# Kernel tuning notes

Measured on AMD Instinct MI355X. Metric: run time of the kernel, lower is better.

Reference implementation:

```python
import jax, jax.numpy as jnp
import numpy as np

B, S, H = 64, 512, 768      # batch, subtokens, BERT hidden
N, E = 128, 1024            # word-nodes per graph, directed edges per graph
GH, FH, L = 128, 256, 2     # gnn_hidden, fc_hidden, num_labels


def setup_inputs() -> dict:
    key = jax.random.key(0)
    ks = jax.random.split(key, 14)
    p = lambda k, shp: 0.02 * jax.random.normal(k, shp, jnp.float32)
    return {
        "last_hidden": jax.random.normal(ks[0], (B, S, H), jnp.float32),
        "submap": jax.random.randint(ks[1], (B, S), 0, N, dtype=jnp.int32),
        "edge_index": jax.random.randint(ks[2], (B, 2, E), 0, N, dtype=jnp.int32),
        "num_nodes": N,
        "wr": p(ks[3], (H,)), "br": jnp.zeros((), jnp.float32),
        "W1": p(ks[4], (H, GH)), "b1": jnp.zeros((GH,), jnp.float32),
        "W2": p(ks[5], (GH, GH)), "b2": jnp.zeros((GH,), jnp.float32),
        "Wf1": p(ks[6], (H + GH, FH)), "bf1": jnp.zeros((FH,), jnp.float32),
        "Wf2": p(ks[7], (FH, L)), "bf2": jnp.zeros((L,), jnp.float32),
    }


def reference(last_hidden, submap, edge_index, num_nodes,
              wr, br, W1, b1, W2, b2, Wf1, bf1, Wf2, bf2):
    Bn, Sn, Hn = last_hidden.shape
    Nn = num_nodes
    BN = Bn * Nn

    # --- per-token rationale gating ---
    gate = jax.nn.sigmoid(jnp.einsum("bsh,h->bs", last_hidden, wr) + br)  # [B,S]
    gated = last_hidden * gate[..., None]                                  # [B,S,H]

    # --- subtoken -> word-node mean pooling (batched segment mean) ---
    offs = (jnp.arange(Bn, dtype=submap.dtype) * Nn)[:, None]
    seg = (submap + offs).reshape(-1)                     # [B*S] global node ids
    flat = gated.reshape(Bn * Sn, Hn)
    sums = jax.ops.segment_sum(flat, seg, num_segments=BN)
    cnts = jax.ops.segment_sum(jnp.ones((Bn * Sn,), flat.dtype), seg, num_segments=BN)
    node_feats = sums / jnp.maximum(cnts, 1.0)[:, None]   # zeros where no subtoken maps

    # --- batched GCN message passing (self-loops + PyG gcn_norm) ---
    eoffs = (jnp.arange(Bn, dtype=edge_index.dtype) * Nn)[:, None]
    src = (edge_index[:, 0, :] + eoffs).reshape(-1)       # [B*E]
    dst = (edge_index[:, 1, :] + eoffs).reshape(-1)
    self_idx = jnp.arange(BN, dtype=src.dtype)
    src_all = jnp.concatenate([src, self_idx])
    dst_all = jnp.concatenate([dst, self_idx])
    deg = jax.ops.segment_sum(jnp.ones_like(src_all, jnp.float32), dst_all, num_segments=BN)
    dinv = jax.lax.rsqrt(deg)                             # deg >= 1 due to self-loops
    norm = dinv[src_all] * dinv[dst_all]                  # [B*E + B*N]

    def gcn_layer(x, W, b):
        h = x @ W                                         # transform first (PyG GCNConv)
        msg = h[src_all] * norm[:, None]
        out = jax.ops.segment_sum(msg, dst_all, num_segments=BN) + b
        return jax.nn.relu(out)                           # relu applied in forward()

    x = gcn_layer(node_feats, W1, b1)
    x = gcn_layer(x, W2, b2)

    # --- graph mean pool, concat with CLS, classifier head (dropout = eval identity) ---
    pooled = x.reshape(Bn, Nn, -1).mean(axis=1)           # [B,GH]
    cls_emb = last_hidden[:, 0, :]                        # [B,H]
    h = jax.nn.relu(jnp.concatenate([cls_emb, pooled], axis=1) @ Wf1 + bf1)
    return h @ Wf2 + bf2                                  # [B,num_labels]
```

## Files before the change

kernel.cpp:

```cpp
#include <hip/hip_runtime.h>
#include <math.h>

#define Bz 64
#define Sz 512
#define Hz 768
#define Nz 128
#define Ez 1024
#define GHz 128
#define FHz 256
#define Lz 2
#define BNz (Bz * Nz)

typedef short bf16x8 __attribute__((ext_vector_type(8)));
typedef float f32x4  __attribute__((ext_vector_type(4)));
typedef unsigned short ushort;

__device__ inline ushort f2b(float f) {
    union { float f; unsigned u; } v; v.f = f;
    return (ushort)((v.u + 0x7FFFu + ((v.u >> 16) & 1u)) >> 16);
}

__global__ __launch_bounds__(256) void k_stage(
        const float* __restrict__ lh, const int* __restrict__ submap,
        const float* __restrict__ wr, const float* __restrict__ br,
        const float* __restrict__ W1, const float* __restrict__ W2,
        const int* __restrict__ ei, const float* __restrict__ Wf1,
        ushort* __restrict__ nfb, ushort* __restrict__ W1T, ushort* __restrict__ W2T,
        int* __restrict__ rowptrG, int* __restrict__ srcsG,
        float* __restrict__ wnG, float* __restrict__ dinvG,
        float* __restrict__ redA_G) {
    int blk = blockIdx.x, t = threadIdx.x;
    __shared__ __align__(16) char arena[17408];

    if (blk < 64) {
        int b = blk;
        float* clsL = (float*)arena;
        float* pA   = (float*)(arena + 3072);
        clsL[t]       = lh[(size_t)b * Sz * Hz + t];
        clsL[t + 256] = lh[(size_t)b * Sz * Hz + t + 256];
        clsL[t + 512] = lh[(size_t)b * Sz * Hz + t + 512];
        __syncthreads();
        int f2 = t & 127, kc = t >> 7;
        const float* Wp = Wf1 + (size_t)(kc * 384) * FHz + f2 * 2;
        const float* ip = clsL + kc * 384;
        float ax = 0.f, ay = 0.f;
        #pragma unroll 8
        for (int k = 0; k < 384; ++k) {
            float iv = ip[k];
            float2 wv = *(const float2*)&Wp[(size_t)k * FHz];
            ax += iv * wv.x; ay += iv * wv.y;
        }
        pA[kc * 256 + f2 * 2]     = ax;
        pA[kc * 256 + f2 * 2 + 1] = ay;
        __syncthreads();
        if (t < 128) {
            float2 o;
            o.x = pA[2 * t]     + pA[256 + 2 * t];
            o.y = pA[2 * t + 1] + pA[256 + 2 * t + 1];
            *(float2*)&redA_G[b * 256 + 2 * t] = o;
        }
        return;
    }
    if (blk < 78) {
        ushort* sT = (ushort*)arena;
        bool isW2 = (blk >= 76);
        int T = isW2 ? (blk - 76) : (blk - 64);
        int k0 = T * 64;
        const float* Wsrc = isW2 ? W2 : W1;
        #pragma unroll
        for (int j = 0; j < 32; ++j) {
            int idx = j * 256 + t;
            int k = idx >> 7, n = idx & 127;
            sT[k * 136 + n] = f2b(Wsrc[(size_t)(k0 + k) * 128 + n]);
        }
        __syncthreads();
        if (isW2) {
            #pragma unroll
            for (int j = 0; j < 32; ++j) {
                int idx = j * 256 + t;
                int n = idx >> 6, k = idx & 63;
                W2T[n * GHz + k0 + k] = sT[k * 136 + n];
            }
        } else {
            #pragma unroll
            for (int j = 0; j < 32; ++j) {
                int idx = j * 256 + t;
                int n = idx >> 6, k = idx & 63;
                W1T[n * Hz + k0 + k] = sT[k * 136 + n];
            }
        }
        return;
    }
    if (blk < 142) {
        int b = blk - 78;
        int*   srcl2 = (int*)arena;
        int*   dstl2 = (int*)(arena + 4096);
        int*   hist  = (int*)(arena + 8192);
        int*   off   = (int*)(arena + 8704);
        int*   rp    = (int*)(arena + 9216);
        float* di    = (float*)(arena + 9732);
        if (t < Nz) { hist[t] = 0; off[t] = 0; }
        __syncthreads();
        #pragma unroll
        for (int j = 0; j < 4; ++j) {
            int e = t + 256 * j;
            int s = ei[b * 2 * Ez + e], d = ei[b * 2 * Ez + Ez + e];
            srcl2[e] = s; dstl2[e] = d;
            atomicAdd(&hist[d], 1);
        }
        __syncthreads();
        if (t < Nz) {
            di[t] = rsqrtf((float)hist[t] + 1.0f);
            dinvG[b * Nz + t] = di[t];
        }
        __syncthreads();
        if (t < 64) {
            int s0 = hist[2 * t], s1 = hist[2 * t + 1];
            int tot = s0 + s1, run = tot;
            #pragma unroll
            for (int o = 1; o < 64; o <<= 1) {
                int v = __shfl_up(run, o);
                if (t >= o) run += v;
            }
            int excl = run - tot;
            rp[2 * t] = excl; rp[2 * t + 1] = excl + s0;
            if (t == 63) rp[Nz] = run;
        }
        __syncthreads();
        #pragma unroll
        for (int j = 0; j < 4; ++j) {
            int e = t + 256 * j;
            int s = srcl2[e], d = dstl2[e];
            int pos = rp[d] + atomicAdd(&off[d], 1);
            srcsG[b * Ez + pos] = s;
            wnG[b * Ez + pos] = di[s] * di[d];
        }
        if (t < Nz) rowptrG[b * (Nz + 1) + t] = rp[t];
        if (t == 0) rowptrG[b * (Nz + 1) + Nz] = rp[Nz];
        return;
    }

    int g = blk - 142;
    int b = g >> 7, n = g & 127;
    int lane = t & 63, wid = t >> 6;
    float* partial = (float*)arena;
    int*   list    = (int*)(arena + 9216);
    int*   lcnt    = (int*)(arena + 11264);
    if (t == 0) *lcnt = 0;
    __syncthreads();
    #pragma unroll
    for (int j = 0; j < 2; ++j) {
        int s = t + 256 * j;
        if (submap[b * Sz + s] == n) { int p = atomicAdd(lcnt, 1); list[p] = s; }
    }
    __syncthreads();
    int cnt = *lcnt;
    float brv = br[0];
    const float* wp = wr + lane * 12;
    float4 w0 = *(const float4*)&wp[0];
    float4 w1 = *(const float4*)&wp[4];
    float4 w2 = *(const float4*)&wp[8];
    float4 a0 = {0,0,0,0}, a1 = {0,0,0,0}, a2 = {0,0,0,0};
    for (int i = wid; i < cnt; i += 4) {
        const float* x = lh + (size_t)(b * Sz + list[i]) * Hz + lane * 12;
        float4 v0 = *(const float4*)&x[0];
        float4 v1 = *(const float4*)&x[4];
        float4 v2 = *(const float4*)&x[8];
        float p = v0.x*w0.x + v0.y*w0.y + v0.z*w0.z + v0.w*w0.w
                + v1.x*w1.x + v1.y*w1.y + v1.z*w1.z + v1.w*w1.w
                + v2.x*w2.x + v2.y*w2.y + v2.z*w2.z + v2.w*w2.w;
        #pragma unroll
        for (int o = 32; o > 0; o >>= 1) p += __shfl_down(p, o);
        float z = __shfl(p, 0) + brv;
        float g2 = 1.0f / (1.0f + __expf(-z));
        a0.x += g2*v0.x; a0.y += g2*v0.y; a0.z += g2*v0.z; a0.w += g2*v0.w;
        a1.x += g2*v1.x; a1.y += g2*v1.y; a1.z += g2*v1.z; a1.w += g2*v1.w;
        a2.x += g2*v2.x; a2.y += g2*v2.y; a2.z += g2*v2.z; a2.w += g2*v2.w;
    }
    if (wid > 0) {
        float* pp = partial + (wid - 1) * Hz + lane * 12;
        *(float4*)&pp[0] = a0; *(float4*)&pp[4] = a1; *(float4*)&pp[8] = a2;
    }
    __syncthreads();
    if (wid == 0) {
        float invc = 1.0f / fmaxf((float)cnt, 1.0f);
        #pragma unroll
        for (int m = 0; m < 3; ++m) {
            const float* pp = partial + m * Hz + lane * 12;
            float4 p0 = *(const float4*)&pp[0];
            float4 p1 = *(const float4*)&pp[4];
            float4 p2 = *(const float4*)&pp[8];
            a0.x += p0.x; a0.y += p0.y; a0.z += p0.z; a0.w += p0.w;
            a1.x += p1.x; a1.y += p1.y; a1.z += p1.z; a1.w += p1.w;
            a2.x += p2.x; a2.y += p2.y; a2.z += p2.z; a2.w += p2.w;
        }
        float o[12];
        o[0]=a0.x*invc; o[1]=a0.y*invc; o[2]=a0.z*invc;  o[3]=a0.w*invc;
        o[4]=a1.x*invc; o[5]=a1.y*invc; o[6]=a1.z*invc;  o[7]=a1.w*invc;
        o[8]=a2.x*invc; o[9]=a2.y*invc; o[10]=a2.z*invc; o[11]=a2.w*invc;
        unsigned* ob = (unsigned*)(nfb + (size_t)(b * Nz + n) * Hz + lane * 12);
        #pragma unroll
        for (int j = 0; j < 6; ++j)
            ob[j] = (unsigned)f2b(o[2*j]) | ((unsigned)f2b(o[2*j+1]) << 16);
    }
}

#define GSP 72
#define O_BS    18432
#define O_HL    36864
#define O_XB    102400
#define O_RP    137216
#define O_SRC   137744
#define O_WN    141840
#define O_DIL   145936
#define O_POOL  146448
#define O_HVEC  146960
__global__ __launch_bounds__(1024) void k_gnn_fused(
        const ushort* __restrict__ nfb, const ushort* __restrict__ W1T,
        const ushort* __restrict__ W2T,
        const int* __restrict__ rowptrG, const int* __restrict__ srcsG,
        const float* __restrict__ wnG, const float* __restrict__ dinvG,
        const float* __restrict__ b1, const float* __restrict__ b2,
        const float* __restrict__ redA_G,
        const float* __restrict__ Wf1, const float* __restrict__ bf1,
        const float* __restrict__ Wf2, const float* __restrict__ bf2,
        float* __restrict__ outG) {
    __shared__ __align__(16) char Lar[147984];
    ushort* As   = (ushort*)(Lar);
    ushort* Bs   = (ushort*)(Lar + O_BS);
    ushort* W2s  = (ushort*)(Lar);
    float*  hLf  = (float*)(Lar + O_HL);
    ushort* xb   = (ushort*)(Lar + O_XB);
    float*  wsum = (float*)(Lar + O_XB);
    float*  redB = (float*)(Lar + O_XB + 8192);
    int*    rp   = (int*)(Lar + O_RP);
    int*    srcl = (int*)(Lar + O_SRC);
    float*  wnl  = (float*)(Lar + O_WN);
    float*  dil  = (float*)(Lar + O_DIL);
    float*  pooledL = (float*)(Lar + O_POOL);
    float*  hvecL   = (float*)(Lar + O_HVEC);
    const float2* hL2 = (const float2*)hLf;

    int b = blockIdx.x;
    int t = threadIdx.x;
    int w = t >> 6, lane = t & 63;
    int q = lane >> 4, l16 = lane & 15;
    int wm = w >> 2, wn2 = w & 3;
    int kq = q * 8;
    int ar = t >> 3, as_ = t & 7;

    const ushort* Ab = nfb + (size_t)b * Nz * Hz;
    uint4 aA, bA, aB, bB;
    aA = *(const uint4*)&Ab[(size_t)ar * Hz + 0  + as_ * 8];
    bA = *(const uint4*)&W1T[(size_t)ar * Hz + 0  + as_ * 8];
    aB = *(const uint4*)&Ab[(size_t)ar * Hz + 64 + as_ * 8];
    bB = *(const uint4*)&W1T[(size_t)ar * Hz + 64 + as_ * 8];
    __builtin_amdgcn_sched_barrier(0);

    if (t < Nz + 1) rp[t] = rowptrG[b * (Nz + 1) + t];
    if (t < Nz) dil[t] = dinvG[b * Nz + t];
    srcl[t] = srcsG[b * Ez + t];
    wnl[t]  = wnG[b * Ez + t];

    f32x4 acc00 = {0,0,0,0}, acc01 = {0,0,0,0}, acc10 = {0,0,0,0}, acc11 = {0,0,0,0};
    auto mfma_tile = [&]() {
        #pragma unroll
        for (int ks = 0; ks < 64; ks += 32) {
            bf16x8 af0 = *(const bf16x8*)&As[(wm * 32 +      l16) * GSP + ks + kq];
            bf16x8 af1 = *(const bf16x8*)&As[(wm * 32 + 16 + l16) * GSP + ks + kq];
            bf16x8 bv0 = *(const bf16x8*)&Bs[(wn2 * 32 +      l16) * GSP + ks + kq];
            bf16x8 bv1 = *(const bf16x8*)&Bs[(wn2 * 32 + 16 + l16) * GSP + ks + kq];
            acc00 = __builtin_amdgcn_mfma_f32_16x16x32_bf16(af0, bv0, acc00, 0, 0, 0);
            acc01 = __builtin_amdgcn_mfma_f32_16x16x32_bf16(af0, bv1, acc01, 0, 0, 0);
            acc10 = __builtin_amdgcn_mfma_f32_16x16x32_bf16(af1, bv0, acc10, 0, 0, 0);
            acc11 = __builtin_amdgcn_mfma_f32_16x16x32_bf16(af1, bv1, acc11, 0, 0, 0);
        }
    };

    for (int k0 = 0; k0 < Hz; k0 += 128) {
        __syncthreads();
        *(uint4*)&As[ar * GSP + as_ * 8] = aA;
        *(uint4*)&Bs[ar * GSP + as_ * 8] = bA;
        if (k0 + 128 < Hz) {
            aA = *(const uint4*)&Ab[(size_t)ar * Hz + k0 + 128 + as_ * 8];
            bA = *(const uint4*)&W1T[(size_t)ar * Hz + k0 + 128 + as_ * 8];
        }
        __builtin_amdgcn_sched_barrier(0);
        __syncthreads();
        mfma_tile();
        __syncthreads();
        *(uint4*)&As[ar * GSP + as_ * 8] = aB;
        *(uint4*)&Bs[ar * GSP + as_ * 8] = bB;
        if (k0 + 192 < Hz) {
            aB = *(const uint4*)&Ab[(size_t)ar * Hz + k0 + 192 + as_ * 8];
            bB = *(const uint4*)&W1T[(size_t)ar * Hz + k0 + 192 + as_ * 8];
        }
        __builtin_amdgcn_sched_barrier(0);
        __syncthreads();
        mfma_tile();
    }
    {
        int c0 = wn2 * 32 + l16, c1 = c0 + 16;
        #pragma unroll
        for (int r = 0; r < 4; ++r) {
            int r0 = (wm * 32 + q * 4 + r) * 128, r1 = r0 + 16 * 128;
            hLf[r0 + (c0 & 63) * 2 + (c0 >> 6)] = acc00[r];
            hLf[r0 + (c1 & 63) * 2 + (c1 >> 6)] = acc01[r];
            hLf[r1 + (c0 & 63) * 2 + (c0 >> 6)] = acc10[r];
            hLf[r1 + (c1 & 63) * 2 + (c1 >> 6)] = acc11[r];
        }
    }
    __syncthreads();

    int n0 = t >> 4, sg = t & 15;
    uint4 w2r0 = *(const uint4*)&W2T[n0 * GHz + sg * 8];
    uint4 w2r1 = *(const uint4*)&W2T[(n0 + 64) * GHz + sg * 8];
    __builtin_amdgcn_sched_barrier(0);

    float bx0 = b1[lane], bx1 = b1[lane + 64];
    for (int d = w; d < Nz; d += 16) {
        float dd = dil[d];
        float2 hv = hL2[d * 64 + lane];
        float a0 = hv.x * dd * dd, a1 = hv.y * dd * dd;
        float c0 = 0.f, c1 = 0.f;
        int i = rp[d], pe = rp[d + 1];
        for (; i + 4 <= pe; i += 4) {
            int s0_ = srcl[i], s1_ = srcl[i+1], s2_ = srcl[i+2], s3_ = srcl[i+3];
            float m0 = wnl[i], m1 = wnl[i+1], m2 = wnl[i+2], m3 = wnl[i+3];
            float2 h0 = hL2[s0_ * 64 + lane], h1 = hL2[s1_ * 64 + lane];
            float2 h2 = hL2[s2_ * 64 + lane], h3 = hL2[s3_ * 64 + lane];
            a0 += h0.x*m0; a1 += h0.y*m0; c0 += h1.x*m1; c1 += h1.y*m1;
            a0 += h2.x*m2; a1 += h2.y*m2; c0 += h3.x*m3; c1 += h3.y*m3;
        }
        for (; i < pe; ++i) {
            int s_ = srcl[i]; float nm = wnl[i];
            float2 h = hL2[s_ * 64 + lane];
            a0 += h.x * nm; a1 += h.y * nm;
        }
        a0 += c0; a1 += c1;
        xb[d * 136 + lane]      = f2b(fmaxf(a0 + bx0, 0.0f));
        xb[d * 136 + lane + 64] = f2b(fmaxf(a1 + bx1, 0.0f));
    }
    __syncthreads();

    *(uint4*)((char*)W2s + n0 * 272 + sg * 16)        = w2r0;
    *(uint4*)((char*)W2s + (n0 + 64) * 272 + sg * 16) = w2r1;
    __syncthreads();

    acc00 = (f32x4){0,0,0,0}; acc01 = (f32x4){0,0,0,0};
    acc10 = (f32x4){0,0,0,0}; acc11 = (f32x4){0,0,0,0};
    #pragma unroll
    for (int ks = 0; ks < GHz; ks += 32) {
        bf16x8 af0 = *(const bf16x8*)&xb[(wm * 32 +      l16) * 136 + ks + kq];
        bf16x8 af1 = *(const bf16x8*)&xb[(wm * 32 + 16 + l16) * 136 + ks + kq];
        bf16x8 bv0 = *(const bf16x8*)&W2s[(wn2 * 32 +      l16) * 136 + ks + kq];
        bf16x8 bv1 = *(const bf16x8*)&W2s[(wn2 * 32 + 16 + l16) * 136 + ks + kq];
        acc00 = __builtin_amdgcn_mfma_f32_16x16x32_bf16(af0, bv0, acc00, 0, 0, 0);
        acc01 = __builtin_amdgcn_mfma_f32_16x16x32_bf16(af0, bv1, acc01, 0, 0, 0);
        acc10 = __builtin_amdgcn_mfma_f32_16x16x32_bf16(af1, bv0, acc10, 0, 0, 0);
        acc11 = __builtin_amdgcn_mfma_f32_16x16x32_bf16(af1, bv1, acc11, 0, 0, 0);
    }
    __syncthreads();
    {
        int c0 = wn2 * 32 + l16, c1 = c0 + 16;
        #pragma unroll
        for (int r = 0; r < 4; ++r) {
            int r0 = (wm * 32 + q * 4 + r) * 128, r1 = r0 + 16 * 128;
            hLf[r0 + (c0 & 63) * 2 + (c0 >> 6)] = acc00[r];
            hLf[r0 + (c1 & 63) * 2 + (c1 >> 6)] = acc01[r];
            hLf[r1 + (c0 & 63) * 2 + (c0 >> 6)] = acc10[r];
            hLf[r1 + (c1 & 63) * 2 + (c1 >> 6)] = acc11[r];
        }
    }
    __syncthreads();

    float by0 = b2[lane], by1 = b2[lane + 64];
    float p0 = 0.0f, p1 = 0.0f;
    for (int d = w; d < Nz; d += 16) {
        float dd = dil[d];
        float2 hv = hL2[d * 64 + lane];
        float a0 = hv.x * dd * dd, a1 = hv.y * dd * dd;
        float c0 = 0.f, c1 = 0.f;
        int i = rp[d], pe = rp[d + 1];
        for (; i + 4 <= pe; i += 4) {
            int s0_ = srcl[i], s1_ = srcl[i+1], s2_ = srcl[i+2], s3_ = srcl[i+3];
            float m0 = wnl[i], m1 = wnl[i+1], m2 = wnl[i+2], m3 = wnl[i+3];
            float2 h0 = hL2[s0_ * 64 + lane], h1 = hL2[s1_ * 64 + lane];
            float2 h2 = hL2[s2_ * 64 + lane], h3 = hL2[s3_ * 64 + lane];
            a0 += h0.x*m0; a1 += h0.y*m0; c0 += h1.x*m1; c1 += h1.y*m1;
            a0 += h2.x*m2; a1 += h2.y*m2; c0 += h3.x*m3; c1 += h3.y*m3;
        }
        for (; i < pe; ++i) {
            int s_ = srcl[i]; float nm = wnl[i];
            float2 h = hL2[s_ * 64 + lane];
            a0 += h.x * nm; a1 += h.y * nm;
        }
        a0 += c0; a1 += c1;
        p0 += fmaxf(a0 + by0, 0.0f);
        p1 += fmaxf(a1 + by1, 0.0f);
    }
    wsum[w * 128 + lane]      = p0;
    wsum[w * 128 + lane + 64] = p1;
    __syncthreads();
    if (t < Nz) {
        float s = 0.0f;
        #pragma unroll
        for (int ww = 0; ww < 16; ++ww) s += wsum[ww * 128 + t];
        pooledL[t] = s * (1.0f / Nz);
    }
    __syncthreads();

    {
        int f2 = t & 127, kc8 = t >> 7;
        const float* Wp = Wf1 + (size_t)(Hz + kc8 * 16) * FHz + f2 * 2;
        const float* ip = pooledL + kc8 * 16;
        float ax = 0.f, ay = 0.f;
        #pragma unroll
        for (int k = 0; k < 16; ++k) {
            float iv = ip[k];
            float2 wv = *(const float2*)&Wp[(size_t)k * FHz];
            ax += iv * wv.x; ay += iv * wv.y;
        }
        redB[kc8 * 256 + f2 * 2]     = ax;
        redB[kc8 * 256 + f2 * 2 + 1] = ay;
    }
    __syncthreads();
    if (t < 128) {
        float sx = bf1[2 * t]     + redA_G[b * 256 + 2 * t];
        float sy = bf1[2 * t + 1] + redA_G[b * 256 + 2 * t + 1];
        #pragma unroll
        for (int m = 0; m < 8; ++m) { sx += redB[m * 256 + 2 * t]; sy += redB[m * 256 + 2 * t + 1]; }
        hvecL[2 * t]     = fmaxf(sx, 0.0f);
        hvecL[2 * t + 1] = fmaxf(sy, 0.0f);
    }
    __syncthreads();
    if (t < 128) {
        int l = t >> 6, j0 = t & 63;
        float s = 0.0f;
        #pragma unroll
        for (int m = 0; m < 4; ++m) s += hvecL[j0 + 64 * m] * Wf2[(j0 + 64 * m) * Lz + l];
        #pragma unroll
        for (int o = 32; o > 0; o >>= 1) s += __shfl_down(s, o);
        if (j0 == 0) outG[b * Lz + l] = s + bf2[l];
    }
}

extern "C" void kernel_launch(void* const* d_in, const int* in_sizes, int n_in,
                              void* d_out, int out_size, void* d_ws, size_t ws_size,
                              hipStream_t stream) {
    const float* lh     = (const float*)d_in[0];
    const int*   submap = (const int*)d_in[1];
    const int*   ei     = (const int*)d_in[2];
    const float* wr  = (const float*)d_in[4];
    const float* br  = (const float*)d_in[5];
    const float* W1  = (const float*)d_in[6];
    const float* b1  = (const float*)d_in[7];
    const float* W2  = (const float*)d_in[8];
    const float* b2  = (const float*)d_in[9];
    const float* Wf1 = (const float*)d_in[10];
    const float* bf1 = (const float*)d_in[11];
    const float* Wf2 = (const float*)d_in[12];
    const float* bf2 = (const float*)d_in[13];
    float* out = (float*)d_out;

    char* p = (char*)d_ws;
    ushort* nfb  = (ushort*)p;  p += (size_t)BNz * Hz * 2;
    ushort* W1T  = (ushort*)p;  p += (size_t)Hz * GHz * 2;
    ushort* W2T  = (ushort*)p;  p += (size_t)GHz * GHz * 2;
    int*    rowptrG = (int*)p;  p += (size_t)Bz * (Nz + 1) * 4;
    int*    srcsG   = (int*)p;  p += (size_t)Bz * Ez * 4;
    float*  wnG     = (float*)p; p += (size_t)Bz * Ez * 4;
    float*  dinvG   = (float*)p; p += (size_t)Bz * Nz * 4;
    float*  redA_G  = (float*)p; p += (size_t)Bz * FHz * 4;

    k_stage<<<142 + 8192, 256, 0, stream>>>(lh, submap, wr, br, W1, W2, ei, Wf1,
                                            nfb, W1T, W2T, rowptrG, srcsG, wnG, dinvG, redA_G);
    k_gnn_fused<<<Bz, 1024, 0, stream>>>(nfb, W1T, W2T, rowptrG, srcsG, wnG, dinvG,
                                         b1, b2, redA_G, Wf1, bf1, Wf2, bf2, out);
}
```

Before: 203.5 us.

## Assign one node per wavefront with ballot scan; deepen GEMM prefetch to three stages

```diff
diff --git a/kernel.cpp b/kernel.cpp
--- a/kernel.cpp
+++ b/kernel.cpp
@@ -141,68 +141,51 @@
     }
 
     int g = blk - 142;
-    int b = g >> 7, n = g & 127;
+    int b = g >> 5, grp = g & 31;
     int lane = t & 63, wid = t >> 6;
-    float* partial = (float*)arena;
-    int*   list    = (int*)(arena + 9216);
-    int*   lcnt    = (int*)(arena + 11264);
-    if (t == 0) *lcnt = 0;
-    __syncthreads();
-    #pragma unroll
-    for (int j = 0; j < 2; ++j) {
-        int s = t + 256 * j;
-        if (submap[b * Sz + s] == n) { int p = atomicAdd(lcnt, 1); list[p] = s; }
-    }
-    __syncthreads();
-    int cnt = *lcnt;
+    int n = grp * 4 + wid;
     float brv = br[0];
     const float* wp = wr + lane * 12;
     float4 w0 = *(const float4*)&wp[0];
     float4 w1 = *(const float4*)&wp[4];
     float4 w2 = *(const float4*)&wp[8];
     float4 a0 = {0,0,0,0}, a1 = {0,0,0,0}, a2 = {0,0,0,0};
-    for (int i = wid; i < cnt; i += 4) {
-        const float* x = lh + (size_t)(b * Sz + list[i]) * Hz + lane * 12;
-        float4 v0 = *(const float4*)&x[0];
-        float4 v1 = *(const float4*)&x[4];
-        float4 v2 = *(const float4*)&x[8];
-        float p = v0.x*w0.x + v0.y*w0.y + v0.z*w0.z + v0.w*w0.w
-                + v1.x*w1.x + v1.y*w1.y + v1.z*w1.z + v1.w*w1.w
-                + v2.x*w2.x + v2.y*w2.y + v2.z*w2.z + v2.w*w2.w;
-        #pragma unroll
-        for (int o = 32; o > 0; o >>= 1) p += __shfl_down(p, o);
-        float z = __shfl(p, 0) + brv;
-        float g2 = 1.0f / (1.0f + __expf(-z));
-        a0.x += g2*v0.x; a0.y += g2*v0.y; a0.z += g2*v0.z; a0.w += g2*v0.w;
-        a1.x += g2*v1.x; a1.y += g2*v1.y; a1.z += g2*v1.z; a1.w += g2*v1.w;
-        a2.x += g2*v2.x; a2.y += g2*v2.y; a2.z += g2*v2.z; a2.w += g2*v2.w;
-    }
-    if (wid > 0) {
-        float* pp = partial + (wid - 1) * Hz + lane * 12;
-        *(float4*)&pp[0] = a0; *(float4*)&pp[4] = a1; *(float4*)&pp[8] = a2;
-    }
-    __syncthreads();
-    if (wid == 0) {
-        float invc = 1.0f / fmaxf((float)cnt, 1.0f);
-        #pragma unroll
-        for (int m = 0; m < 3; ++m) {
-            const float* pp = partial + m * Hz + lane * 12;
-            float4 p0 = *(const float4*)&pp[0];
-            float4 p1 = *(const float4*)&pp[4];
-            float4 p2 = *(const float4*)&pp[8];
-            a0.x += p0.x; a0.y += p0.y; a0.z += p0.z; a0.w += p0.w;
-            a1.x += p1.x; a1.y += p1.y; a1.z += p1.z; a1.w += p1.w;
-            a2.x += p2.x; a2.y += p2.y; a2.z += p2.z; a2.w += p2.w;
-        }
-        float o[12];
-        o[0]=a0.x*invc; o[1]=a0.y*invc; o[2]=a0.z*invc;  o[3]=a0.w*invc;
-        o[4]=a1.x*invc; o[5]=a1.y*invc; o[6]=a1.z*invc;  o[7]=a1.w*invc;
-        o[8]=a2.x*invc; o[9]=a2.y*invc; o[10]=a2.z*invc; o[11]=a2.w*invc;
-        unsigned* ob = (unsigned*)(nfb + (size_t)(b * Nz + n) * Hz + lane * 12);
-        #pragma unroll
-        for (int j = 0; j < 6; ++j)
-            ob[j] = (unsigned)f2b(o[2*j]) | ((unsigned)f2b(o[2*j+1]) << 16);
-    }
+    int cnt = 0;
+    const int* smp = submap + (size_t)b * Sz;
+    #pragma unroll
+    for (int s0 = 0; s0 < Sz; s0 += 64) {
+        int sm = smp[s0 + lane];
+        unsigned long long m = __ballot(sm == n);
+        while (m) {
+            int bit = __ffsll((unsigned long long)m) - 1;
+            m &= m - 1;
+            int s = s0 + bit;
+            const float* x = lh + (size_t)(b * Sz + s) * Hz + lane * 12;
+            float4 v0 = *(const float4*)&x[0];
+            float4 v1 = *(const float4*)&x[4];
+            float4 v2 = *(const float4*)&x[8];
+            float p = v0.x*w0.x + v0.y*w0.y + v0.z*w0.z + v0.w*w0.w
+                    + v1.x*w1.x + v1.y*w1.y + v1.z*w1.z + v1.w*w1.w
+                    + v2.x*w2.x + v2.y*w2.y + v2.z*w2.z + v2.w*w2.w;
+            #pragma unroll
+            for (int o = 32; o > 0; o >>= 1) p += __shfl_down(p, o);
+            float z = __shfl(p, 0) + brv;
+            float gte = 1.0f / (1.0f + __expf(-z));
+            a0.x += gte*v0.x; a0.y += gte*v0.y; a0.z += gte*v0.z; a0.w += gte*v0.w;
+            a1.x += gte*v1.x; a1.y += gte*v1.y; a1.z += gte*v1.z; a1.w += gte*v1.w;
+            a2.x += gte*v2.x; a2.y += gte*v2.y; a2.z += gte*v2.z; a2.w += gte*v2.w;
+            ++cnt;
+        }
+    }
+    float invc = 1.0f / fmaxf((float)cnt, 1.0f);
+    float o[12];
+    o[0]=a0.x*invc; o[1]=a0.y*invc; o[2]=a0.z*invc;  o[3]=a0.w*invc;
+    o[4]=a1.x*invc; o[5]=a1.y*invc; o[6]=a1.z*invc;  o[7]=a1.w*invc;
+    o[8]=a2.x*invc; o[9]=a2.y*invc; o[10]=a2.z*invc; o[11]=a2.w*invc;
+    unsigned* ob = (unsigned*)(nfb + (size_t)(b * Nz + n) * Hz + lane * 12);
+    #pragma unroll
+    for (int j = 0; j < 6; ++j)
+        ob[j] = (unsigned)f2b(o[2*j]) | ((unsigned)f2b(o[2*j+1]) << 16);
 }
 
 #define GSP 72
@@ -250,11 +233,13 @@
     int ar = t >> 3, as_ = t & 7;
 
     const ushort* Ab = nfb + (size_t)b * Nz * Hz;
-    uint4 aA, bA, aB, bB;
-    aA = *(const uint4*)&Ab[(size_t)ar * Hz + 0  + as_ * 8];
-    bA = *(const uint4*)&W1T[(size_t)ar * Hz + 0  + as_ * 8];
-    aB = *(const uint4*)&Ab[(size_t)ar * Hz + 64 + as_ * 8];
-    bB = *(const uint4*)&W1T[(size_t)ar * Hz + 64 + as_ * 8];
+    uint4 aA, bA, aB, bB, aC, bC;
+    aA = *(const uint4*)&Ab[(size_t)ar * Hz + 0   + as_ * 8];
+    bA = *(const uint4*)&W1T[(size_t)ar * Hz + 0   + as_ * 8];
+    aB = *(const uint4*)&Ab[(size_t)ar * Hz + 64  + as_ * 8];
+    bB = *(const uint4*)&W1T[(size_t)ar * Hz + 64  + as_ * 8];
+    aC = *(const uint4*)&Ab[(size_t)ar * Hz + 128 + as_ * 8];
+    bC = *(const uint4*)&W1T[(size_t)ar * Hz + 128 + as_ * 8];
     __builtin_amdgcn_sched_barrier(0);
 
     if (t < Nz + 1) rp[t] = rowptrG[b * (Nz + 1) + t];
@@ -277,13 +262,13 @@
         }
     };
 
-    for (int k0 = 0; k0 < Hz; k0 += 128) {
+    for (int k0 = 0; k0 < Hz; k0 += 192) {
         __syncthreads();
         *(uint4*)&As[ar * GSP + as_ * 8] = aA;
         *(uint4*)&Bs[ar * GSP + as_ * 8] = bA;
-        if (k0 + 128 < Hz) {
-            aA = *(const uint4*)&Ab[(size_t)ar * Hz + k0 + 128 + as_ * 8];
-            bA = *(const uint4*)&W1T[(size_t)ar * Hz + k0 + 128 + as_ * 8];
+        if (k0 + 192 < Hz) {
+            aA = *(const uint4*)&Ab[(size_t)ar * Hz + k0 + 192 + as_ * 8];
+            bA = *(const uint4*)&W1T[(size_t)ar * Hz + k0 + 192 + as_ * 8];
         }
         __builtin_amdgcn_sched_barrier(0);
         __syncthreads();
@@ -291,9 +276,19 @@
         __syncthreads();
         *(uint4*)&As[ar * GSP + as_ * 8] = aB;
         *(uint4*)&Bs[ar * GSP + as_ * 8] = bB;
-        if (k0 + 192 < Hz) {
-            aB = *(const uint4*)&Ab[(size_t)ar * Hz + k0 + 192 + as_ * 8];
-            bB = *(const uint4*)&W1T[(size_t)ar * Hz + k0 + 192 + as_ * 8];
+        if (k0 + 256 < Hz) {
+            aB = *(const uint4*)&Ab[(size_t)ar * Hz + k0 + 256 + as_ * 8];
+            bB = *(const uint4*)&W1T[(size_t)ar * Hz + k0 + 256 + as_ * 8];
+        }
+        __builtin_amdgcn_sched_barrier(0);
+        __syncthreads();
+        mfma_tile();
+        __syncthreads();
+        *(uint4*)&As[ar * GSP + as_ * 8] = aC;
+        *(uint4*)&Bs[ar * GSP + as_ * 8] = bC;
+        if (k0 + 320 < Hz) {
+            aC = *(const uint4*)&Ab[(size_t)ar * Hz + k0 + 320 + as_ * 8];
+            bC = *(const uint4*)&W1T[(size_t)ar * Hz + k0 + 320 + as_ * 8];
         }
         __builtin_amdgcn_sched_barrier(0);
         __syncthreads();
@@ -473,7 +468,7 @@
     float*  dinvG   = (float*)p; p += (size_t)Bz * Nz * 4;
     float*  redA_G  = (float*)p; p += (size_t)Bz * FHz * 4;
 
-    k_stage<<<142 + 8192, 256, 0, stream>>>(lh, submap, wr, br, W1, W2, ei, Wf1,
+    k_stage<<<142 + 2048, 256, 0, stream>>>(lh, submap, wr, br, W1, W2, ei, Wf1,
                                             nfb, W1T, W2T, rowptrG, srcsG, wnG, dinvG, redA_G);
     k_gnn_fused<<<Bz, 1024, 0, stream>>>(nfb, W1T, W2T, rowptrG, srcsG, wnG, dinvG,
                                          b1, b2, redA_G, Wf1, bf1, Wf2, bf2, out);
```

Measured after the change: 208.2 us. 2.4% more time.
